# Kernel optimization log

Hardware: AMD Instinct MI355X
Metric: run time of the kernel (lower is better)

## Reference

```python
import jax, jax.numpy as jnp
import numpy as np

B, L, D_MODEL = 4, 4096, 128
D_INNER, D_STATE, DT_RANK, D_CONV = 256, 16, 8, 4
EPS = 1e-5


def setup_inputs() -> dict:
    key = jax.random.key(0)
    ks = jax.random.split(key, 10)
    s = lambda *sh: 0.02
    inp = {
        'x': jax.random.normal(ks[0], (B, L, D_MODEL), jnp.float32),
        'norm_w': jnp.ones((D_MODEL,), jnp.float32),
        # Linear weights stored as (in, out) so y = x @ W
        'in_proj_w': jax.random.normal(ks[1], (D_MODEL, 2 * D_INNER), jnp.float32) * 0.02,
        'conv_w': jax.random.normal(ks[2], (D_INNER, D_CONV), jnp.float32) * 0.2,
        'conv_b': jnp.zeros((D_INNER,), jnp.float32),
        'x_proj_w': jax.random.normal(ks[3], (D_INNER, DT_RANK + 2 * D_STATE), jnp.float32) * 0.02,
        'dt_proj_w': jax.random.normal(ks[4], (DT_RANK, D_INNER), jnp.float32) * 0.1,
        'dt_proj_b': jnp.zeros((D_INNER,), jnp.float32),
        'A_log': jnp.log(jnp.tile(jnp.arange(1, D_STATE + 1, dtype=jnp.float32)[None, :], (D_INNER, 1))),
        'D': jnp.ones((D_INNER,), jnp.float32),
        'out_proj_w': jax.random.normal(ks[5], (D_INNER, D_MODEL), jnp.float32) * 0.02,
    }
    return inp


def _mamba_block(x, norm_w, in_proj_w, conv_w, conv_b, x_proj_w,
                 dt_proj_w, dt_proj_b, A_log, D, out_proj_w):
    b, l, d = x.shape
    # RMSNorm
    h = x * jax.lax.rsqrt(jnp.mean(x * x, axis=-1, keepdims=True) + EPS) * norm_w
    # in_proj -> split into x path and residual gate
    xr = h @ in_proj_w                      # (b, l, 2*d_inner)
    xi, res = jnp.split(xr, 2, axis=-1)
    # depthwise causal conv1d over time
    xc = jnp.transpose(xi, (0, 2, 1))       # (b, d_inner, l)
    kernel = conv_w[:, None, :]             # (d_inner, 1, d_conv)
    xc = jax.lax.conv_general_dilated(
        xc, kernel, window_strides=(1,), padding=[(D_CONV - 1, 0)],
        feature_group_count=D_INNER,
        dimension_numbers=('NCH', 'OIH', 'NCH')) + conv_b[None, :, None]
    xc = jnp.transpose(xc, (0, 2, 1))       # (b, l, d_inner)
    xc = jax.nn.silu(xc)
    # SSM parameterization
    A = -jnp.exp(A_log.astype(jnp.float32))           # (d_inner, n)
    x_dbl = xc @ x_proj_w                              # (b, l, dt_rank + 2n)
    delta = x_dbl[..., :DT_RANK]
    Bmat = x_dbl[..., DT_RANK:DT_RANK + D_STATE]       # (b, l, n)
    Cmat = x_dbl[..., DT_RANK + D_STATE:]              # (b, l, n)
    delta = jax.nn.softplus(delta @ dt_proj_w + dt_proj_b)  # (b, l, d_inner)
    # discretize
    deltaA = jnp.exp(jnp.einsum('bld,dn->bldn', delta, A))  # (b, l, d_inner, n)
    deltaB_u = delta[..., None] * Bmat[:, :, None, :] * xc[..., None]
    # selective scan over time (lax.scan replaces the Python loop)
    def step(s, inputs):
        dA_t, dBu_t, C_t = inputs
        s = dA_t * s + dBu_t                     # (b, d_inner, n)
        y_t = jnp.einsum('bdn,bn->bd', s, C_t)   # (b, d_inner)
        return s, y_t
    s0 = jnp.zeros((b, D_INNER, D_STATE), xc.dtype)
    scan_in = (jnp.transpose(deltaA, (1, 0, 2, 3)),
               jnp.transpose(deltaB_u, (1, 0, 2, 3)),
               jnp.transpose(Cmat, (1, 0, 2)))
    _, ys = jax.lax.scan(step, s0, scan_in)      # (l, b, d_inner)
    y = jnp.transpose(ys, (1, 0, 2)) + xc * D    # (b, l, d_inner)
    y = y * jax.nn.silu(res)
    return y @ out_proj_w + x                    # residual add


def reference(x, norm_w, in_proj_w, conv_w, conv_b, x_proj_w,
              dt_proj_w, dt_proj_b, A_log, D, out_proj_w):
    return _mamba_block(x, norm_w, in_proj_w, conv_w, conv_b, x_proj_w,
                        dt_proj_w, dt_proj_b, A_log, D, out_proj_w)
```

## Files before the change

### kernel.cpp

```cpp
#include <hip/hip_runtime.h>
#include <math.h>

#define B_    4
#define L_    4096
#define DM    128
#define DI    256
#define DS    16
#define DTR   8
#define XPN   (DTR + 2*DS)
#define NB    (DI + 2*DS)
#define M_    (B_*L_)
#define CHUNK 32
#define NC    (L_/CHUNK)
#define LOG2E 1.4426950408889634f
#define PREP_N (512*128 + NB*DI + DM*DI)

typedef __attribute__((ext_vector_type(8))) short bf16x8;
typedef __attribute__((ext_vector_type(4))) float f32x4;
typedef unsigned short ushort_t;

__device__ __forceinline__ ushort_t f2bf(float f) {
  unsigned int u = __float_as_uint(f);
  u += 0x7FFFu + ((u >> 16) & 1u);
  return (ushort_t)(u >> 16);
}
__device__ __forceinline__ float bf2f(ushort_t u) {
  return __uint_as_float(((unsigned int)u) << 16);
}

__global__ __launch_bounds__(256) void prep_rms_kernel(const float* __restrict__ x,
                                                       const float* __restrict__ nw,
                                                       const float* __restrict__ inW,
                                                       const float* __restrict__ Wx,
                                                       const float* __restrict__ Wdt,
                                                       const float* __restrict__ outw,
                                                       ushort_t* __restrict__ xbf,
                                                       ushort_t* __restrict__ inWt,
                                                       ushort_t* __restrict__ WbigT,
                                                       ushort_t* __restrict__ outWt) {
  if (blockIdx.x < M_ / 4) {
    int row  = blockIdx.x * 4 + (threadIdx.x >> 6);
    int lane = threadIdx.x & 63;
    const float* xp = x + (size_t)row * DM;
    float v0 = xp[lane], v1 = xp[lane + 64];
    float s = v0 * v0 + v1 * v1;
    #pragma unroll
    for (int off = 32; off > 0; off >>= 1) s += __shfl_xor(s, off);
    float r = rsqrtf(s / DM + 1e-5f);
    ushort_t* op = xbf + (size_t)row * DM;
    op[lane]      = f2bf(v0 * r * nw[lane]);
    op[lane + 64] = f2bf(v1 * r * nw[lane + 64]);
    return;
  }
  int g = (blockIdx.x - M_ / 4) * 256 + threadIdx.x;
  if (g < 512 * 128) {
    int n = g >> 7, k = g & 127;
    inWt[g] = f2bf(inW[k * 512 + n]);
  } else if (g < 512 * 128 + NB * DI) {
    int q = g - 512 * 128;
    int c = q >> 8, k = q & 255;
    float v;
    if (c < DI) {
      v = 0.f;
      #pragma unroll
      for (int j = 0; j < DTR; ++j) v = fmaf(Wx[k * XPN + j], Wdt[j * DI + c], v);
    } else {
      v = Wx[k * XPN + DTR + (c - DI)];
    }
    WbigT[q] = f2bf(v);
  } else if (g < PREP_N) {
    int q = g - (512 * 128 + NB * DI);
    int n = q >> 8, k = q & 255;
    outWt[q] = f2bf(outw[k * DM + n]);
  }
}

__global__ __launch_bounds__(256) void g1_conv_kernel(const ushort_t* __restrict__ A,
                                                      const ushort_t* __restrict__ Wt,
                                                      const float* __restrict__ cw,
                                                      const float* __restrict__ cb,
                                                      ushort_t* __restrict__ xcbf,
                                                      ushort_t* __restrict__ resbf) {
  constexpr int KK = 128, NT = 4;
  __shared__ __align__(16) char smem_raw[35648];
  ushort_t (*Asm)[145][8] = (ushort_t (*)[145][8])smem_raw;
  ushort_t (*Bx)[65][8]   = (ushort_t (*)[65][8])(smem_raw + 18560);
  ushort_t (*Br)[65][8]   = (ushort_t (*)[65][8])(smem_raw + 26880);
  float* T = (float*)smem_raw;
  const int tid  = threadIdx.x;
  const int wave = tid >> 6, lane = tid & 63;
  const int quad = lane >> 4, l16 = lane & 15;
  const int row0 = blockIdx.x * 128;
  const int by   = blockIdx.y;
  const int c0x  = by * 64;
  const int c0r  = 256 + by * 64;
  const bool zpad = (row0 & (L_ - 1)) == 0;
  f32x4 ax[2][NT], ar[2][NT], acc2[NT];
  #pragma unroll
  for (int mt = 0; mt < 2; ++mt)
    #pragma unroll
    for (int nt = 0; nt < NT; ++nt) {
      ax[mt][nt] = (f32x4){0.f, 0.f, 0.f, 0.f};
      ar[mt][nt] = (f32x4){0.f, 0.f, 0.f, 0.f};
    }
  #pragma unroll
  for (int nt = 0; nt < NT; ++nt) acc2[nt] = (f32x4){0.f, 0.f, 0.f, 0.f};

  for (int k0 = 0; k0 < KK; k0 += 64) {
    #pragma unroll
    for (int i = 0; i < 5; ++i) {
      int q = tid + i * 256;
      if (i < 4 || tid < 128) {
        int m = q >> 3, kb = q & 7;
        bf16x8 v = {0, 0, 0, 0, 0, 0, 0, 0};
        if (!(zpad && m < 16))
          v = *(const bf16x8*)(A + (size_t)(row0 - 16 + m) * KK + k0 + kb * 8);
        *(bf16x8*)(&Asm[kb][m][0]) = v;
      }
    }
    #pragma unroll
    for (int i = 0; i < 2; ++i) {
      int q = tid + i * 256;
      int n = q >> 3, kb = q & 7;
      *(bf16x8*)(&Bx[kb][n][0]) =
          *(const bf16x8*)(Wt + (size_t)(c0x + n) * KK + k0 + kb * 8);
    }
    #pragma unroll
    for (int i = 0; i < 2; ++i) {
      int q = tid + i * 256;
      int n = q >> 3, kb = q & 7;
      *(bf16x8*)(&Br[kb][n][0]) =
          *(const bf16x8*)(Wt + (size_t)(c0r + n) * KK + k0 + kb * 8);
    }
    __syncthreads();
    #pragma unroll
    for (int ks = 0; ks < 2; ++ks) {
      bf16x8 af[2], bx[NT], br[NT];
      #pragma unroll
      for (int mt = 0; mt < 2; ++mt)
        af[mt] = *(const bf16x8*)(&Asm[ks * 4 + quad][16 + wave * 32 + mt * 16 + l16][0]);
      #pragma unroll
      for (int nt = 0; nt < NT; ++nt) {
        bx[nt] = *(const bf16x8*)(&Bx[ks * 4 + quad][nt * 16 + l16][0]);
        br[nt] = *(const bf16x8*)(&Br[ks * 4 + quad][nt * 16 + l16][0]);
      }
      #pragma unroll
      for (int mt = 0; mt < 2; ++mt)
        #pragma unroll
        for (int nt = 0; nt < NT; ++nt) {
          ax[mt][nt] = __builtin_amdgcn_mfma_f32_16x16x32_bf16(af[mt], bx[nt],
                                                               ax[mt][nt], 0, 0, 0);
          ar[mt][nt] = __builtin_amdgcn_mfma_f32_16x16x32_bf16(af[mt], br[nt],
                                                               ar[mt][nt], 0, 0, 0);
        }
      if (wave == 0) {
        bf16x8 ab = *(const bf16x8*)(&Asm[ks * 4 + quad][l16][0]);
        #pragma unroll
        for (int nt = 0; nt < NT; ++nt)
          acc2[nt] = __builtin_amdgcn_mfma_f32_16x16x32_bf16(ab, bx[nt],
                                                             acc2[nt], 0, 0, 0);
      }
    }
    __syncthreads();
  }

  #pragma unroll
  for (int mt = 0; mt < 2; ++mt)
    #pragma unroll
    for (int nt = 0; nt < NT; ++nt) {
      int col   = c0x + nt * 16 + l16;
      int rbase = row0 + wave * 32 + mt * 16 + quad * 4;
      #pragma unroll
      for (int r = 0; r < 4; ++r)
        resbf[(size_t)(rbase + r) * DI + col] = f2bf(ar[mt][nt][r]);
    }

  #pragma unroll
  for (int mt = 0; mt < 2; ++mt)
    #pragma unroll
    for (int nt = 0; nt < NT; ++nt)
      #pragma unroll
      for (int r = 0; r < 4; ++r)
        T[(3 + wave * 32 + mt * 16 + quad * 4 + r) * 68 + nt * 16 + l16] =
            ax[mt][nt][r];
  if (wave == 0 && quad == 3) {
    #pragma unroll
    for (int nt = 0; nt < NT; ++nt)
      #pragma unroll
      for (int r = 1; r < 4; ++r)
        T[(r - 1) * 68 + nt * 16 + l16] = acc2[nt][r];
  }
  __syncthreads();
  {
    const int c   = tid & 63;
    const int R0  = (tid >> 6) * 32;
    const int dch = c0x + c;
    float4 w4   = *(const float4*)(cw + dch * 4);
    float bias  = cb[dch];
    float t0 = T[(R0 + 0) * 68 + c];
    float t1 = T[(R0 + 1) * 68 + c];
    float t2 = T[(R0 + 2) * 68 + c];
    for (int rr = 0; rr < 32; ++rr) {
      float t3 = T[(R0 + rr + 3) * 68 + c];
      float s = fmaf(w4.x, t0, fmaf(w4.y, t1, fmaf(w4.z, t2, fmaf(w4.w, t3, bias))));
      float v = s / (1.f + __expf(-s));
      xcbf[(size_t)(row0 + R0 + rr) * DI + dch] = f2bf(v);
      t0 = t1; t1 = t2; t2 = t3;
    }
  }
}

__global__ __launch_bounds__(512, 4) void scanA_kernel(
    const ushort_t* __restrict__ xcbf, const ushort_t* __restrict__ WbigT,
    const float* __restrict__ bdt, const float* __restrict__ Alog,
    ushort_t* __restrict__ deltab, ushort_t* __restrict__ Bmb,
    ushort_t* __restrict__ Cmb, float2* __restrict__ PS) {
  __shared__ __align__(16) ushort_t Asm[32][33][8];
  __shared__ float T[32][257];
  __shared__ float Bs[32][17], Cs[32][17];
  const int tid  = threadIdx.x;
  const int wave = tid >> 6, lane = tid & 63;
  const int quad = lane >> 4, l16 = lane & 15;
  const int b = blockIdx.x >> 7, c = blockIdx.x & (NC - 1);
  const size_t rowbase = (size_t)b * L_ + (size_t)c * CHUNK;
  const int d  = (wave << 5) | (lane & 31);
  const int nh = lane >> 5;
  const int n0 = nh * 8;

  {
    int m = tid & 31, kb = tid >> 5;
    *(bf16x8*)(&Asm[kb][m][0]) =
        *(const bf16x8*)(xcbf + (rowbase + m) * DI + kb * 8);
    *(bf16x8*)(&Asm[kb + 16][m][0]) =
        *(const bf16x8*)(xcbf + (rowbase + m) * DI + (kb + 16) * 8);
  }
  __syncthreads();

  for (int tp = wave; tp < 36; tp += 8) {
    int mt = tp / 18, nt = tp % 18;
    f32x4 acc = {0.f, 0.f, 0.f, 0.f};
    #pragma unroll
    for (int ks = 0; ks < 8; ++ks) {
      bf16x8 af = *(const bf16x8*)(&Asm[ks * 4 + quad][mt * 16 + l16][0]);
      bf16x8 bf = *(const bf16x8*)(WbigT + (size_t)(nt * 16 + l16) * DI + ks * 32 + quad * 8);
      acc = __builtin_amdgcn_mfma_f32_16x16x32_bf16(af, bf, acc, 0, 0, 0);
    }
    int row = mt * 16 + quad * 4;
    if (nt < 16) {
      int col = nt * 16 + l16;
      float bb = bdt[col];
      #pragma unroll
      for (int r = 0; r < 4; ++r) {
        float v = acc[r] + bb;
        T[row + r][col] = (v > 20.f) ? v : log1pf(__expf(v));
      }
    } else if (nt == 16) {
      #pragma unroll
      for (int r = 0; r < 4; ++r) Bs[row + r][l16] = acc[r];
    } else {
      #pragma unroll
      for (int r = 0; r < 4; ++r) Cs[row + r][l16] = acc[r];
    }
  }
  __syncthreads();

  #pragma unroll
  for (int i = 0; i < 8; ++i) {
    int idx2 = tid + i * 512;
    int row = idx2 >> 7, cp = idx2 & 127;
    unsigned int pk = (unsigned int)f2bf(T[row][2 * cp]) |
                      ((unsigned int)f2bf(T[row][2 * cp + 1]) << 16);
    *(unsigned int*)(deltab + (rowbase + row) * DI + 2 * cp) = pk;
  }
  {
    int row = tid >> 4, n = tid & 15;
    Bmb[rowbase * DS + tid] = f2bf(Bs[row][n]);
    Cmb[rowbase * DS + tid] = f2bf(Cs[row][n]);
  }

  float c0 = -__expf(Alog[d * DS]) * LOG2E;
  float aln[8];
  #pragma unroll
  for (int j = 0; j < 8; ++j) aln[j] = -__expf(Alog[d * DS + n0 + j]) * LOG2E;
  bool geom = true;
  #pragma unroll
  for (int j = 0; j < 8; ++j)
    geom = geom && (fabsf(aln[j] - (n0 + j + 1) * c0) <= 1e-3f * fabsf(aln[j]));

  float P[8], S[8];
  #pragma unroll
  for (int j = 0; j < 8; ++j) { P[j] = 1.f; S[j] = 0.f; }
  for (int t = 0; t < CHUNK; ++t) {
    float dl = T[t][d];
    float xv = bf2f(Asm[d >> 3][t][d & 7]);
    float du = dl * xv;
    if (geom) {
      float e1 = exp2f(dl * c0);
      float a;
      if (nh) { float e2 = e1 * e1, e4 = e2 * e2; a = e4 * e4 * e1; }
      else a = e1;
      #pragma unroll
      for (int j = 0; j < 8; ++j) {
        P[j] *= a;
        S[j] = fmaf(a, S[j], du * Bs[t][n0 + j]);
        a *= e1;
      }
    } else {
      #pragma unroll
      for (int j = 0; j < 8; ++j) {
        float a = exp2f(dl * aln[j]);
        P[j] *= a;
        S[j] = fmaf(a, S[j], du * Bs[t][n0 + j]);
      }
    }
  }
  size_t ob = ((size_t)(b * NC + c) << 12) + ((nh * 256 + d) << 3);
  float4* p4 = (float4*)(PS + ob);
  p4[0] = make_float4(P[0], S[0], P[1], S[1]);
  p4[1] = make_float4(P[2], S[2], P[3], S[3]);
  p4[2] = make_float4(P[4], S[4], P[5], S[5]);
  p4[3] = make_float4(P[6], S[6], P[7], S[7]);
}

__global__ __launch_bounds__(64) void scanB_kernel(const float2* __restrict__ PS,
                                                   float* __restrict__ sinit) {
  int g  = blockIdx.x * 64 + threadIdx.x;
  int b  = g >> 12;
  int dn = g & 4095;
  float s = 0.f;
  #pragma unroll 16
  for (int c = 0; c < NC; ++c) {
    size_t idx = ((size_t)(b * NC + c) << 12) + dn;
    sinit[idx] = s;
    float2 v = PS[idx];
    s = fmaf(v.x, s, v.y);
  }
}

__global__ __launch_bounds__(512, 4) void scanC_kernel(
    const ushort_t* __restrict__ deltab, const ushort_t* __restrict__ xcbf,
    const ushort_t* __restrict__ Bmb, const ushort_t* __restrict__ Cmb,
    const float* __restrict__ Alog, const float* __restrict__ Dp,
    const ushort_t* __restrict__ resbf, const float* __restrict__ sinit,
    const ushort_t* __restrict__ outWt, const float* __restrict__ x,
    float* __restrict__ out) {
  __shared__ float Bs[32][17], Cs[32][17];
  __shared__ __align__(16) ushort_t y2s[32][264];
  const int tid  = threadIdx.x;
  const int wave = tid >> 6, lane = tid & 63;
  const int quad = lane >> 4, l16 = lane & 15;
  const int b = blockIdx.x >> 7, c = blockIdx.x & (NC - 1);
  const size_t rowbase = (size_t)b * L_ + (size_t)c * CHUNK;
  const int d  = (wave << 5) | (lane & 31);
  const int nh = lane >> 5;
  const int n0 = nh * 8;
  {
    int row = tid >> 4, n = tid & 15;
    Bs[row][n] = bf2f(Bmb[rowbase * DS + tid]);
    Cs[row][n] = bf2f(Cmb[rowbase * DS + tid]);
  }
  float c0 = -__expf(Alog[d * DS]) * LOG2E;
  float aln[8];
  #pragma unroll
  for (int j = 0; j < 8; ++j) aln[j] = -__expf(Alog[d * DS + n0 + j]) * LOG2E;
  bool geom = true;
  #pragma unroll
  for (int j = 0; j < 8; ++j)
    geom = geom && (fabsf(aln[j] - (n0 + j + 1) * c0) <= 1e-3f * fabsf(aln[j]));
  const float Dd = Dp[d];
  float S[8];
  {
    size_t ib = ((size_t)(b * NC + c) << 12) + ((nh * 256 + d) << 3);
    float4 v0 = *(const float4*)(sinit + ib);
    float4 v1 = *(const float4*)(sinit + ib + 4);
    S[0] = v0.x; S[1] = v0.y; S[2] = v0.z; S[3] = v0.w;
    S[4] = v1.x; S[5] = v1.y; S[6] = v1.z; S[7] = v1.w;
  }
  __syncthreads();
  for (int t = 0; t < CHUNK; ++t) {
    float dl = bf2f(deltab[(rowbase + t) * DI + d]);
    float xv = bf2f(xcbf[(rowbase + t) * DI + d]);
    float du = dl * xv;
    float y = 0.f;
    if (geom) {
      float e1 = exp2f(dl * c0);
      float a;
      if (nh) { float e2 = e1 * e1, e4 = e2 * e2; a = e4 * e4 * e1; }
      else a = e1;
      #pragma unroll
      for (int j = 0; j < 8; ++j) {
        S[j] = fmaf(a, S[j], du * Bs[t][n0 + j]);
        y = fmaf(S[j], Cs[t][n0 + j], y);
        a *= e1;
      }
    } else {
      #pragma unroll
      for (int j = 0; j < 8; ++j) {
        float a = exp2f(dl * aln[j]);
        S[j] = fmaf(a, S[j], du * Bs[t][n0 + j]);
        y = fmaf(S[j], Cs[t][n0 + j], y);
      }
    }
    float yo = __shfl_xor(y, 32);
    if (nh == 0) {
      float rv = bf2f(resbf[(rowbase + t) * DI + d]);
      float yt = y + yo + xv * Dd;
      float sil = rv / (1.f + __expf(-rv));
      y2s[t][d] = f2bf(yt * sil);
    }
  }
  __syncthreads();
  #pragma unroll
  for (int mt = 0; mt < 2; ++mt) {
    f32x4 acc = {0.f, 0.f, 0.f, 0.f};
    #pragma unroll
    for (int ks = 0; ks < 8; ++ks) {
      bf16x8 af = *(const bf16x8*)(&y2s[mt * 16 + l16][ks * 32 + quad * 8]);
      bf16x8 bf = *(const bf16x8*)(outWt + (size_t)(wave * 16 + l16) * DI + ks * 32 + quad * 8);
      acc = __builtin_amdgcn_mfma_f32_16x16x32_bf16(af, bf, acc, 0, 0, 0);
    }
    int col = wave * 16 + l16;
    size_t rb = rowbase + mt * 16 + quad * 4;
    #pragma unroll
    for (int r = 0; r < 4; ++r)
      out[(rb + r) * DM + col] = acc[r] + x[(rb + r) * DM + col];
  }
}

extern "C" void kernel_launch(void* const* d_in, const int* in_sizes, int n_in,
                              void* d_out, int out_size, void* d_ws, size_t ws_size,
                              hipStream_t stream) {
  const float* x      = (const float*)d_in[0];
  const float* norm_w = (const float*)d_in[1];
  const float* inW    = (const float*)d_in[2];
  const float* convw  = (const float*)d_in[3];
  const float* convb  = (const float*)d_in[4];
  const float* xprojw = (const float*)d_in[5];
  const float* dtw    = (const float*)d_in[6];
  const float* dtb    = (const float*)d_in[7];
  const float* alog   = (const float*)d_in[8];
  const float* Dp     = (const float*)d_in[9];
  const float* outw   = (const float*)d_in[10];
  float* out = (float*)d_out;

  const size_t CS = (size_t)B_ * NC * DI * DS;
  float2* PS    = (float2*)d_ws;
  float* sinit  = (float*)(PS + CS);
  ushort_t* bfbase = (ushort_t*)(sinit + CS);
  ushort_t* xbf    = bfbase;
  ushort_t* xcbf   = xbf + (size_t)M_ * DM;
  ushort_t* resbf  = xcbf + (size_t)M_ * DI;
  ushort_t* deltab = resbf + (size_t)M_ * DI;
  ushort_t* Bmb    = deltab + (size_t)M_ * DI;
  ushort_t* Cmb    = Bmb + (size_t)M_ * DS;
  ushort_t* inWt   = Cmb + (size_t)M_ * DS;
  ushort_t* WbigT  = inWt + 512 * 128;
  ushort_t* outWt  = WbigT + NB * DI;

  prep_rms_kernel<<<M_ / 4 + (PREP_N + 255) / 256, 256, 0, stream>>>(
      x, norm_w, inW, xprojw, dtw, outw, xbf, inWt, WbigT, outWt);
  g1_conv_kernel<<<dim3(M_ / 128, 4), 256, 0, stream>>>(
      xbf, inWt, convw, convb, xcbf, resbf);
  scanA_kernel<<<B_ * NC, 512, 0, stream>>>(
      xcbf, WbigT, dtb, alog, deltab, Bmb, Cmb, PS);
  scanB_kernel<<<(B_ * DI * DS) / 64, 64, 0, stream>>>(PS, sinit);
  scanC_kernel<<<B_ * NC, 512, 0, stream>>>(
      deltab, xcbf, Bmb, Cmb, alog, Dp, resbf, sinit, outWt, x, out);
}
```

Baseline: 169.1 us.

## Fuse inter-chunk prefix scan into scanA via last-block atomic counter

Removes the separate scanB kernel launch. Each scanA block bumps a per-batch atomic counter after writing its chunk summary, and the last block for a batch runs the sequential carry propagation across all chunks, writing sinit. Counters are reset in the prep kernel. This saves a launch and its idle gap, but the serial scan now runs in only four blocks of 512 threads, each walking 128 chunks, on the critical path.

```diff
diff --git a/kernel.cpp b/kernel.cpp
--- a/kernel.cpp
+++ b/kernel.cpp
@@ -37,8 +37,10 @@
                                                        ushort_t* __restrict__ xbf,
                                                        ushort_t* __restrict__ inWt,
                                                        ushort_t* __restrict__ WbigT,
-                                                       ushort_t* __restrict__ outWt) {
+                                                       ushort_t* __restrict__ outWt,
+                                                       unsigned int* __restrict__ counters) {
   if (blockIdx.x < M_ / 4) {
+    if (blockIdx.x == 0 && threadIdx.x < B_) counters[threadIdx.x] = 0u;
     int row  = blockIdx.x * 4 + (threadIdx.x >> 6);
     int lane = threadIdx.x & 63;
     const float* xp = x + (size_t)row * DM;
@@ -214,10 +216,12 @@
     const ushort_t* __restrict__ xcbf, const ushort_t* __restrict__ WbigT,
     const float* __restrict__ bdt, const float* __restrict__ Alog,
     ushort_t* __restrict__ deltab, ushort_t* __restrict__ Bmb,
-    ushort_t* __restrict__ Cmb, float2* __restrict__ PS) {
+    ushort_t* __restrict__ Cmb, float2* __restrict__ PS,
+    float* __restrict__ sinit, unsigned int* __restrict__ counters) {
   __shared__ __align__(16) ushort_t Asm[32][33][8];
   __shared__ float T[32][257];
   __shared__ float Bs[32][17], Cs[32][17];
+  __shared__ int lastFlag;
   const int tid  = threadIdx.x;
   const int wave = tid >> 6, lane = tid & 63;
   const int quad = lane >> 4, l16 = lane & 15;
@@ -320,20 +324,32 @@
   p4[1] = make_float4(P[2], S[2], P[3], S[3]);
   p4[2] = make_float4(P[4], S[4], P[5], S[5]);
   p4[3] = make_float4(P[6], S[6], P[7], S[7]);
-}
-
-__global__ __launch_bounds__(64) void scanB_kernel(const float2* __restrict__ PS,
-                                                   float* __restrict__ sinit) {
-  int g  = blockIdx.x * 64 + threadIdx.x;
-  int b  = g >> 12;
-  int dn = g & 4095;
-  float s = 0.f;
-  #pragma unroll 16
-  for (int c = 0; c < NC; ++c) {
-    size_t idx = ((size_t)(b * NC + c) << 12) + dn;
-    sinit[idx] = s;
-    float2 v = PS[idx];
-    s = fmaf(v.x, s, v.y);
+
+  __syncthreads();
+  if (tid == 0) {
+    __threadfence();
+    unsigned int prev = atomicAdd(&counters[b], 1u);
+    lastFlag = (prev == NC - 1);
+  }
+  __syncthreads();
+  if (!lastFlag) return;
+  __threadfence();
+
+  {
+    const int slot = tid * 8;
+    float s0 = 0.f, s1 = 0.f, s2 = 0.f, s3 = 0.f,
+          s4 = 0.f, s5 = 0.f, s6 = 0.f, s7 = 0.f;
+    for (int cc = 0; cc < NC; ++cc) {
+      size_t base = ((size_t)(b * NC + cc) << 12) + slot;
+      *(float4*)(sinit + base)     = make_float4(s0, s1, s2, s3);
+      *(float4*)(sinit + base + 4) = make_float4(s4, s5, s6, s7);
+      const float4* q = (const float4*)(PS + base);
+      float4 a0 = q[0], a1 = q[1], a2 = q[2], a3 = q[3];
+      s0 = fmaf(a0.x, s0, a0.y); s1 = fmaf(a0.z, s1, a0.w);
+      s2 = fmaf(a1.x, s2, a1.y); s3 = fmaf(a1.z, s3, a1.w);
+      s4 = fmaf(a2.x, s4, a2.y); s5 = fmaf(a2.z, s5, a2.w);
+      s6 = fmaf(a3.x, s6, a3.y); s7 = fmaf(a3.z, s7, a3.w);
+    }
   }
 }
 
@@ -456,14 +472,14 @@
   ushort_t* inWt   = Cmb + (size_t)M_ * DS;
   ushort_t* WbigT  = inWt + 512 * 128;
   ushort_t* outWt  = WbigT + NB * DI;
+  unsigned int* counters = (unsigned int*)(outWt + DM * DI);
 
   prep_rms_kernel<<<M_ / 4 + (PREP_N + 255) / 256, 256, 0, stream>>>(
-      x, norm_w, inW, xprojw, dtw, outw, xbf, inWt, WbigT, outWt);
+      x, norm_w, inW, xprojw, dtw, outw, xbf, inWt, WbigT, outWt, counters);
   g1_conv_kernel<<<dim3(M_ / 128, 4), 256, 0, stream>>>(
       xbf, inWt, convw, convb, xcbf, resbf);
   scanA_kernel<<<B_ * NC, 512, 0, stream>>>(
-      xcbf, WbigT, dtb, alog, deltab, Bmb, Cmb, PS);
-  scanB_kernel<<<(B_ * DI * DS) / 64, 64, 0, stream>>>(PS, sinit);
+      xcbf, WbigT, dtb, alog, deltab, Bmb, Cmb, PS, sinit, counters);
   scanC_kernel<<<B_ * NC, 512, 0, stream>>>(
       deltab, xcbf, Bmb, Cmb, alog, Dp, resbf, sinit, outWt, x, out);
 }
```

Measured after the change: 373.4 us. +120.8%, slower.
